# Optimization experiments

Hardware: AMD Instinct MI355X
Metric: run time of the kernel (lower is better)

Reference implementation:

```python
import jax, jax.numpy as jnp
import numpy as np

B, R, H, Q, D = 16, 400, 8, 64, 1200  # BatchSize, ROIs, heads, q, BOLDs
THRESH_INIT = 0.01

def setup_inputs() -> dict:
    key = jax.random.key(0)
    k1, k2, k3, k4, k5 = jax.random.split(key, 5)
    s = 1.0 / np.sqrt(D)
    return {
        "x": jax.random.normal(k1, (B, R, D), dtype=jnp.float32),
        "Wq": jax.random.normal(k2, (D, H * Q), dtype=jnp.float32) * s,
        "bq": jax.random.normal(k3, (H * Q,), dtype=jnp.float32) * 0.01,
        "Wk": jax.random.normal(k4, (D, H * Q), dtype=jnp.float32) * s,
        "bk": jax.random.normal(k5, (H * Q,), dtype=jnp.float32) * 0.01,
        "threshold": jnp.ones((), dtype=jnp.float32),
    }

def reference(x, Wq, bq, Wk, bk, threshold):
    # Q,K projections: [B,R,H*Q] -> [B,R,H,Q]
    q = (x @ Wq + bq).reshape(B, R, H, Q)
    k = (x @ Wk + bk).reshape(B, R, H, Q)
    # QK^T per head: [B,H,R,R]
    rel = jnp.einsum("bihq,bjhq->bhij", q, k) / jnp.float32(Q)
    rel = jax.nn.softmax(rel, axis=-1)
    # threshold-subtract + relu sparsification (learned scalar, init 0.01)
    rel = jax.nn.relu(rel - threshold * THRESH_INIT)
    return rel
```

## Files before the change

### kernel.cpp

```cpp
#include <hip/hip_runtime.h>
#include <stdint.h>

#define DPAD 1216
#define MROWS 6400

typedef float f32x4 __attribute__((ext_vector_type(4)));
typedef __bf16 bf16x8 __attribute__((ext_vector_type(8)));
typedef __attribute__((address_space(3))) uint8_t as3_u8;
typedef __attribute__((address_space(1))) uint8_t as1_u8;

__device__ __forceinline__ void gload_lds16(const void* g, void* l) {
  __builtin_amdgcn_global_load_lds((as1_u8*)g, (as3_u8*)l, 16, 0, 0);
}

__global__ void cvt_x(const float* __restrict__ x, __bf16* __restrict__ xb) {
  const int id = blockIdx.x * 256 + threadIdx.x;
  const int row = id / 152;
  const int c = id - row * 152;
  const int col = c * 8;
  bf16x8 v;
  if (col < 1200) {
    const float4* p = (const float4*)(x + row * 1200 + col);
    const float4 f0 = p[0], f1 = p[1];
    v[0] = (__bf16)f0.x; v[1] = (__bf16)f0.y; v[2] = (__bf16)f0.z; v[3] = (__bf16)f0.w;
    v[4] = (__bf16)f1.x; v[5] = (__bf16)f1.y; v[6] = (__bf16)f1.z; v[7] = (__bf16)f1.w;
  } else {
#pragma unroll
    for (int i = 0; i < 8; ++i) v[i] = (__bf16)0.0f;
  }
  *(bf16x8*)(xb + (size_t)row * DPAD + col) = v;
}

__global__ void cvt_w(const float* __restrict__ wq, const float* __restrict__ wk,
                      __bf16* __restrict__ wt) {
  const int id = blockIdx.x * 256 + threadIdx.x;
  const int n = id / 152;
  const int c = id - n * 152;
  const int k0 = c * 8;
  const float* src = (n < 512) ? (wq + n) : (wk + (n - 512));
  bf16x8 v;
#pragma unroll
  for (int i = 0; i < 8; ++i) {
    const int k = k0 + i;
    v[i] = (k < 1200) ? (__bf16)src[(size_t)k * 512] : (__bf16)0.0f;
  }
  *(bf16x8*)(wt + (size_t)n * DPAD + k0) = v;
}

__global__ __launch_bounds__(256) void gemm_qk(const __bf16* __restrict__ xb,
                                               const __bf16* __restrict__ wt,
                                               const float* __restrict__ bq,
                                               const float* __restrict__ bk,
                                               __bf16* __restrict__ qk) {
  __shared__ __bf16 As[128 * 32];
  __shared__ __bf16 Bs[128 * 32];
  const int m0 = blockIdx.x * 128;
  const int n0 = blockIdx.y * 128;
  const int t = threadIdx.x;
  const int lane = t & 63;
  const int wid = t >> 6;
  const int wr = wid >> 1, wc = wid & 1;
  const int lrow = lane & 15, lk = lane >> 4;

  f32x4 acc[4][4];
#pragma unroll
  for (int i = 0; i < 4; ++i)
#pragma unroll
    for (int j = 0; j < 4; ++j) acc[i][j] = (f32x4){0.f, 0.f, 0.f, 0.f};

  for (int k0 = 0; k0 < DPAD; k0 += 32) {
#pragma unroll
    for (int it = 0; it < 2; ++it) {
      const int id = it * 256 + t;
      const int row = id >> 2, cc = id & 3;
      gload_lds16(xb + (size_t)(m0 + row) * DPAD + k0 + cc * 8, (char*)As + id * 16);
      gload_lds16(wt + (size_t)(n0 + row) * DPAD + k0 + cc * 8, (char*)Bs + id * 16);
    }
    __syncthreads();
    bf16x8 a[4], bfr[4];
#pragma unroll
    for (int i = 0; i < 4; ++i)
      a[i] = *(const bf16x8*)(As + (wr * 64 + i * 16 + lrow) * 32 + lk * 8);
#pragma unroll
    for (int i = 0; i < 4; ++i)
      bfr[i] = *(const bf16x8*)(Bs + (wc * 64 + i * 16 + lrow) * 32 + lk * 8);
#pragma unroll
    for (int mi = 0; mi < 4; ++mi)
#pragma unroll
      for (int ni = 0; ni < 4; ++ni)
        acc[mi][ni] = __builtin_amdgcn_mfma_f32_16x16x32_bf16(a[mi], bfr[ni], acc[mi][ni], 0, 0, 0);
    __syncthreads();
  }
#pragma unroll
  for (int mi = 0; mi < 4; ++mi) {
#pragma unroll
    for (int ni = 0; ni < 4; ++ni) {
      const int gr0 = m0 + wr * 64 + mi * 16 + lk * 4;
      const int gc = n0 + wc * 64 + ni * 16 + lrow;
      const float bias = (gc < 512) ? bq[gc] : bk[gc - 512];
#pragma unroll
      for (int r = 0; r < 4; ++r)
        qk[(size_t)(gr0 + r) * 1024 + gc] = (__bf16)(acc[mi][ni][r] + bias);
    }
  }
}

__global__ __launch_bounds__(256) void attn(const __bf16* __restrict__ qk,
                                            const float* __restrict__ thr_p,
                                            float* __restrict__ out) {
  __shared__ __bf16 klds[400 * 64];
  __shared__ __bf16 qlds[16 * 64];
  __shared__ float slds[16 * 404];
  const int bh = blockIdx.y;
  const int b = bh >> 3;
  const int h = bh & 7;
  const int r0 = blockIdx.x * 16;
  const int t = threadIdx.x;
  const int lane = t & 63;
  const int wid = t >> 6;
  const __bf16* kbase = qk + (size_t)(b * 400) * 1024 + 512 + h * 64;
  const __bf16* qbase = qk + (size_t)(b * 400 + r0) * 1024 + h * 64;

#pragma unroll
  for (int it = 0; it < 12; ++it) {
    const int id = it * 256 + t;
    const int row = id >> 3, c = id & 7;
    const int csw = c ^ (row & 7);
    gload_lds16(kbase + (size_t)row * 1024 + csw * 8, (char*)klds + id * 16);
  }
  if (wid < 2) {
    const int id = 3072 + t;
    const int row = id >> 3, c = id & 7;
    const int csw = c ^ (row & 7);
    gload_lds16(kbase + (size_t)row * 1024 + csw * 8, (char*)klds + id * 16);
    const int qrow = t >> 3, qc = t & 7;
    gload_lds16(qbase + (size_t)qrow * 1024 + qc * 8, (char*)qlds + t * 16);
  }
  __syncthreads();

  const int lrow = lane & 15, lk = lane >> 4;
  bf16x8 aq[2];
#pragma unroll
  for (int kk = 0; kk < 2; ++kk)
    aq[kk] = *(const bf16x8*)(qlds + lrow * 64 + kk * 32 + lk * 8);

  for (int jt = wid; jt < 25; jt += 4) {
    f32x4 acc = (f32x4){0.f, 0.f, 0.f, 0.f};
#pragma unroll
    for (int kk = 0; kk < 2; ++kk) {
      const int krow = jt * 16 + lrow;
      const int cwant = kk * 4 + lk;
      const int csw = cwant ^ (krow & 7);
      const bf16x8 bkf = *(const bf16x8*)(klds + krow * 64 + csw * 8);
      acc = __builtin_amdgcn_mfma_f32_16x16x32_bf16(aq[kk], bkf, acc, 0, 0, 0);
    }
    const int scol = jt * 16 + lrow;
#pragma unroll
    for (int r = 0; r < 4; ++r)
      slds[(lk * 4 + r) * 404 + scol] = acc[r] * 0.015625f;
  }
  __syncthreads();

  const int row = t >> 4, c = t & 15;
  const float thr = thr_p[0] * 0.01f;
  float vals[25];
  float m = -1e30f;
#pragma unroll
  for (int j = 0; j < 25; ++j) {
    vals[j] = slds[row * 404 + j * 16 + c];
    m = fmaxf(m, vals[j]);
  }
#pragma unroll
  for (int off = 8; off >= 1; off >>= 1) m = fmaxf(m, __shfl_xor(m, off, 16));
  float sum = 0.f;
#pragma unroll
  for (int j = 0; j < 25; ++j) {
    vals[j] = __expf(vals[j] - m);
    sum += vals[j];
  }
#pragma unroll
  for (int off = 8; off >= 1; off >>= 1) sum += __shfl_xor(sum, off, 16);
  const float inv = 1.0f / sum;
  float* orow = out + ((size_t)bh * 400 + r0 + row) * 400;
#pragma unroll
  for (int j = 0; j < 25; ++j) {
    const float p = vals[j] * inv - thr;
    orow[j * 16 + c] = p > 0.f ? p : 0.f;
  }
}

extern "C" void kernel_launch(void* const* d_in, const int* in_sizes, int n_in,
                              void* d_out, int out_size, void* d_ws, size_t ws_size,
                              hipStream_t stream) {
  const float* x   = (const float*)d_in[0];
  const float* Wq  = (const float*)d_in[1];
  const float* bq  = (const float*)d_in[2];
  const float* Wk  = (const float*)d_in[3];
  const float* bk  = (const float*)d_in[4];
  const float* thr = (const float*)d_in[5];
  char* ws = (char*)d_ws;
  __bf16* xb = (__bf16*)ws;
  __bf16* wt = (__bf16*)(ws + 15564800);
  __bf16* qk = (__bf16*)(ws + 18055168);
  float* out = (float*)d_out;

  cvt_x<<<dim3(3800), dim3(256), 0, stream>>>(x, xb);
  cvt_w<<<dim3(608), dim3(256), 0, stream>>>(Wq, Wk, wt);
  gemm_qk<<<dim3(50, 8), dim3(256), 0, stream>>>(xb, wt, bq, bk, qk);
  attn<<<dim3(25, 128), dim3(256), 0, stream>>>(qk, thr, out);
}
```

Baseline: 78.75 us.

## Deepen GEMM K-tile, remap blocks across XCDs, load attn Q/K directly from global

The QK projection GEMM now stages 64-wide K slices per iteration, which halves the number of barrier pairs, and uses a 1D grid remapped so consecutive blocks land on different XCDs that share N tiles. The attention kernel drops its LDS staging of K and Q and reads MFMA fragments straight from global memory through cache. This shrinks LDS use and raises occupancy, at the risk of uncoalesced global fragment loads and repeated K reads from L2. The score buffer padding is also removed, so LDS bank conflicts on it may return.

```diff
diff --git a/kernel.cpp b/kernel.cpp
--- a/kernel.cpp
+++ b/kernel.cpp
@@ -52,10 +52,12 @@
                                                const float* __restrict__ bq,
                                                const float* __restrict__ bk,
                                                __bf16* __restrict__ qk) {
-  __shared__ __bf16 As[128 * 32];
-  __shared__ __bf16 Bs[128 * 32];
-  const int m0 = blockIdx.x * 128;
-  const int n0 = blockIdx.y * 128;
+  __shared__ __bf16 As[128 * 64];
+  __shared__ __bf16 Bs[128 * 64];
+  const int bid = blockIdx.x;
+  const int wg = (bid & 7) * 50 + (bid >> 3);
+  const int n0 = (wg / 50) * 128;
+  const int m0 = (wg % 50) * 128;
   const int t = threadIdx.x;
   const int lane = t & 63;
   const int wid = t >> 6;
@@ -68,27 +70,30 @@
 #pragma unroll
     for (int j = 0; j < 4; ++j) acc[i][j] = (f32x4){0.f, 0.f, 0.f, 0.f};
 
-  for (int k0 = 0; k0 < DPAD; k0 += 32) {
+  for (int k0 = 0; k0 < DPAD; k0 += 64) {
 #pragma unroll
-    for (int it = 0; it < 2; ++it) {
+    for (int it = 0; it < 4; ++it) {
       const int id = it * 256 + t;
-      const int row = id >> 2, cc = id & 3;
+      const int row = id >> 3, cc = id & 7;
       gload_lds16(xb + (size_t)(m0 + row) * DPAD + k0 + cc * 8, (char*)As + id * 16);
       gload_lds16(wt + (size_t)(n0 + row) * DPAD + k0 + cc * 8, (char*)Bs + id * 16);
     }
     __syncthreads();
-    bf16x8 a[4], bfr[4];
+    bf16x8 a[4][2], bfr[4][2];
 #pragma unroll
     for (int i = 0; i < 4; ++i)
-      a[i] = *(const bf16x8*)(As + (wr * 64 + i * 16 + lrow) * 32 + lk * 8);
 #pragma unroll
-    for (int i = 0; i < 4; ++i)
-      bfr[i] = *(const bf16x8*)(Bs + (wc * 64 + i * 16 + lrow) * 32 + lk * 8);
+      for (int kk = 0; kk < 2; ++kk) {
+        a[i][kk]   = *(const bf16x8*)(As + (wr * 64 + i * 16 + lrow) * 64 + kk * 32 + lk * 8);
+        bfr[i][kk] = *(const bf16x8*)(Bs + (wc * 64 + i * 16 + lrow) * 64 + kk * 32 + lk * 8);
+      }
 #pragma unroll
-    for (int mi = 0; mi < 4; ++mi)
+    for (int kk = 0; kk < 2; ++kk)
 #pragma unroll
-      for (int ni = 0; ni < 4; ++ni)
-        acc[mi][ni] = __builtin_amdgcn_mfma_f32_16x16x32_bf16(a[mi], bfr[ni], acc[mi][ni], 0, 0, 0);
+      for (int mi = 0; mi < 4; ++mi)
+#pragma unroll
+        for (int ni = 0; ni < 4; ++ni)
+          acc[mi][ni] = __builtin_amdgcn_mfma_f32_16x16x32_bf16(a[mi][kk], bfr[ni][kk], acc[mi][ni], 0, 0, 0);
     __syncthreads();
   }
 #pragma unroll
@@ -108,9 +113,7 @@
 __global__ __launch_bounds__(256) void attn(const __bf16* __restrict__ qk,
                                             const float* __restrict__ thr_p,
                                             float* __restrict__ out) {
-  __shared__ __bf16 klds[400 * 64];
-  __shared__ __bf16 qlds[16 * 64];
-  __shared__ float slds[16 * 404];
+  __shared__ float slds[16 * 400];
   const int bh = blockIdx.y;
   const int b = bh >> 3;
   const int h = bh & 7;
@@ -118,46 +121,26 @@
   const int t = threadIdx.x;
   const int lane = t & 63;
   const int wid = t >> 6;
+  const int lrow = lane & 15, lk = lane >> 4;
   const __bf16* kbase = qk + (size_t)(b * 400) * 1024 + 512 + h * 64;
   const __bf16* qbase = qk + (size_t)(b * 400 + r0) * 1024 + h * 64;
 
-#pragma unroll
-  for (int it = 0; it < 12; ++it) {
-    const int id = it * 256 + t;
-    const int row = id >> 3, c = id & 7;
-    const int csw = c ^ (row & 7);
-    gload_lds16(kbase + (size_t)row * 1024 + csw * 8, (char*)klds + id * 16);
-  }
-  if (wid < 2) {
-    const int id = 3072 + t;
-    const int row = id >> 3, c = id & 7;
-    const int csw = c ^ (row & 7);
-    gload_lds16(kbase + (size_t)row * 1024 + csw * 8, (char*)klds + id * 16);
-    const int qrow = t >> 3, qc = t & 7;
-    gload_lds16(qbase + (size_t)qrow * 1024 + qc * 8, (char*)qlds + t * 16);
-  }
-  __syncthreads();
-
-  const int lrow = lane & 15, lk = lane >> 4;
   bf16x8 aq[2];
 #pragma unroll
   for (int kk = 0; kk < 2; ++kk)
-    aq[kk] = *(const bf16x8*)(qlds + lrow * 64 + kk * 32 + lk * 8);
+    aq[kk] = *(const bf16x8*)(qbase + (size_t)lrow * 1024 + kk * 32 + lk * 8);
 
   for (int jt = wid; jt < 25; jt += 4) {
     f32x4 acc = (f32x4){0.f, 0.f, 0.f, 0.f};
 #pragma unroll
     for (int kk = 0; kk < 2; ++kk) {
-      const int krow = jt * 16 + lrow;
-      const int cwant = kk * 4 + lk;
-      const int csw = cwant ^ (krow & 7);
-      const bf16x8 bkf = *(const bf16x8*)(klds + krow * 64 + csw * 8);
+      const bf16x8 bkf = *(const bf16x8*)(kbase + (size_t)(jt * 16 + lrow) * 1024 + kk * 32 + lk * 8);
       acc = __builtin_amdgcn_mfma_f32_16x16x32_bf16(aq[kk], bkf, acc, 0, 0, 0);
     }
     const int scol = jt * 16 + lrow;
 #pragma unroll
     for (int r = 0; r < 4; ++r)
-      slds[(lk * 4 + r) * 404 + scol] = acc[r] * 0.015625f;
+      slds[(lk * 4 + r) * 400 + scol] = acc[r] * 0.015625f;
   }
   __syncthreads();
 
@@ -167,7 +150,7 @@
   float m = -1e30f;
 #pragma unroll
   for (int j = 0; j < 25; ++j) {
-    vals[j] = slds[row * 404 + j * 16 + c];
+    vals[j] = slds[row * 400 + j * 16 + c];
     m = fmaxf(m, vals[j]);
   }
 #pragma unroll
@@ -206,6 +189,6 @@
 
   cvt_x<<<dim3(3800), dim3(256), 0, stream>>>(x, xb);
   cvt_w<<<dim3(608), dim3(256), 0, stream>>>(Wq, Wk, wt);
-  gemm_qk<<<dim3(50, 8), dim3(256), 0, stream>>>(xb, wt, bq, bk, qk);
+  gemm_qk<<<dim3(400), dim3(256), 0, stream>>>(xb, wt, bq, bk, qk);
   attn<<<dim3(25, 128), dim3(256), 0, stream>>>(qk, thr, out);
 }
```

Result: slower. 85.20 us (+8.2%).
